# Kernel optimization log

Measured on AMD Instinct MI355X. Metric: run time of the kernel, lower is better.

## Reference

```python
import jax, jax.numpy as jnp
import numpy as np

N_NODES = 100000
N_EDGES = 3200000
D_NODE = 128
D_EDGE = 16


def setup_inputs() -> dict:
    key = jax.random.key(0)
    k1, k2, k3, k4, k5, k6, k7 = jax.random.split(key, 7)
    nodes = jax.random.normal(k1, (N_NODES, D_NODE), dtype=jnp.float32)
    edges = jax.random.normal(k2, (N_EDGES, D_EDGE), dtype=jnp.float32)
    senders = jax.random.randint(k3, (N_EDGES,), 0, N_NODES, dtype=jnp.int32)
    receivers = jax.random.randint(k4, (N_EDGES,), 0, N_NODES, dtype=jnp.int32)
    w_node = jax.random.normal(k5, (), dtype=jnp.float32)
    w_edge = jax.random.normal(k6, (), dtype=jnp.float32)
    b_node = jax.random.normal(k7, (), dtype=jnp.float32)
    return {
        "nodes": nodes,
        "edges": edges,
        "senders": senders,
        "receivers": receivers,
        "w_node": w_node,
        "w_edge": w_edge,
        "b_node": b_node,
    }


def reference(nodes, edges, senders, receivers, w_node, w_edge, b_node):
    # gather sender node scalar feature (column 0): [E]
    sender_vals = nodes[senders, 0]
    edge_vals = edges[:, 0]  # [E]
    # per-edge message: scalar mult-add
    messages = w_edge * edge_vals + w_node * sender_vals  # [E]
    # scatter-add into receivers: [N]
    agg = jax.ops.segment_sum(messages, receivers, num_segments=nodes.shape[0])
    return w_node * nodes[:, 0] + agg + b_node
```

## Files before the change

kernel.cpp:

```cpp
#include <hip/hip_runtime.h>

#define N_NODES 100000
#define N_EDGES 3200000
#define D_NODE 128
#define D_EDGE 16

#define NB 80
#define SLICE_E (N_EDGES / NB)

#define K1_THREADS 512
#define K1_EPT 8
#define K1_TILE (K1_THREADS * K1_EPT)

#define WS_X      0
#define WS_MSG    102400
#define WS_PART   (102400 + N_EDGES)
#define WS_TOTAL  (WS_PART + NB * N_NODES)

__global__ void tmp_k0_extract(const float* __restrict__ nodes,
                               float* __restrict__ x) {
    int i = blockIdx.x * blockDim.x + threadIdx.x;
    if (i < N_NODES) x[i] = nodes[(size_t)i * D_NODE];
}

__global__ __launch_bounds__(K1_THREADS) void tmp_k1_messages(
        const float* __restrict__ x,
        const float* __restrict__ edges,
        const int*   __restrict__ senders,
        const float* __restrict__ w_node,
        const float* __restrict__ w_edge,
        float* __restrict__ msg) {
    const float wn = w_node[0];
    const float we = w_edge[0];
    const int tile = blockIdx.x * K1_TILE;
#pragma unroll
    for (int j = 0; j < K1_EPT; ++j) {
        int e = tile + j * K1_THREADS + (int)threadIdx.x;
        if (e < N_EDGES) {
            float ev = __builtin_nontemporal_load(edges + (size_t)e * D_EDGE);
            int   s  = senders[e];
            msg[e] = we * ev + wn * x[s];
        }
    }
}

__global__ __launch_bounds__(1024) void tmp_k2_accum(
        const float* __restrict__ msg,
        const int*   __restrict__ receivers,
        float* __restrict__ partials,
        int range_floats) {
    extern __shared__ float acc[];
    const int lo   = blockIdx.y * range_floats;
    int span = N_NODES - lo; if (span > range_floats) span = range_floats;
    const unsigned uspan = (unsigned)span;
    const int slice = blockIdx.x;

    for (int i = threadIdx.x; i < span; i += 1024) acc[i] = 0.f;
    __syncthreads();

    const int start = slice * SLICE_E;
    const int end   = start + SLICE_E;
    for (int e = start + (int)threadIdx.x * 4; e < end; e += 1024 * 4) {
        int4   r = *(const int4*)(receivers + e);
        float4 m = *(const float4*)(msg + e);
        unsigned ux = (unsigned)(r.x - lo);
        unsigned uy = (unsigned)(r.y - lo);
        unsigned uz = (unsigned)(r.z - lo);
        unsigned uw = (unsigned)(r.w - lo);
        if (ux < uspan) atomicAdd(&acc[ux], m.x);
        if (uy < uspan) atomicAdd(&acc[uy], m.y);
        if (uz < uspan) atomicAdd(&acc[uz], m.z);
        if (uw < uspan) atomicAdd(&acc[uw], m.w);
    }
    __syncthreads();

    float* dst = partials + (size_t)slice * N_NODES + lo;
    for (int i = threadIdx.x * 4; i < span; i += 1024 * 4) {
        *(float4*)(dst + i) = *(const float4*)(acc + i);
    }
}

__global__ void tmp_k3_reduce(const float* __restrict__ x,
                              const float* __restrict__ partials,
                              const float* __restrict__ w_node,
                              const float* __restrict__ b_node,
                              float* __restrict__ out) {
    int i = blockIdx.x * blockDim.x + threadIdx.x;
    if (i >= N_NODES) return;
    float s = w_node[0] * x[i] + b_node[0];
    const float* p = partials + i;
#pragma unroll 4
    for (int b = 0; b < NB; ++b) s += p[(size_t)b * N_NODES];
    out[i] = s;
}

__global__ void tmp_init_out(const float* __restrict__ nodes,
                             const float* __restrict__ w_node,
                             const float* __restrict__ b_node,
                             float* __restrict__ out) {
    int i = blockIdx.x * blockDim.x + threadIdx.x;
    if (i < N_NODES) out[i] = w_node[0] * nodes[(size_t)i * D_NODE] + b_node[0];
}

__global__ void tmp_edge_scatter_direct(const float* __restrict__ nodes,
                                        const float* __restrict__ edges,
                                        const int*   __restrict__ senders,
                                        const int*   __restrict__ receivers,
                                        const float* __restrict__ w_node,
                                        const float* __restrict__ w_edge,
                                        float* __restrict__ out) {
    const float wn = w_node[0];
    const float we = w_edge[0];
    int base = (blockIdx.x * blockDim.x + threadIdx.x) * 4;
    if (base + 3 < N_EDGES) {
        int4 s = *(const int4*)(senders + base);
        int4 r = *(const int4*)(receivers + base);
        atomicAdd(&out[r.x], we * edges[(size_t)(base + 0) * D_EDGE] + wn * nodes[(size_t)s.x * D_NODE]);
        atomicAdd(&out[r.y], we * edges[(size_t)(base + 1) * D_EDGE] + wn * nodes[(size_t)s.y * D_NODE]);
        atomicAdd(&out[r.z], we * edges[(size_t)(base + 2) * D_EDGE] + wn * nodes[(size_t)s.z * D_NODE]);
        atomicAdd(&out[r.w], we * edges[(size_t)(base + 3) * D_EDGE] + wn * nodes[(size_t)s.w * D_NODE]);
    } else {
        for (int e = base; e < N_EDGES; ++e) {
            atomicAdd(&out[receivers[e]],
                      we * edges[(size_t)e * D_EDGE] + wn * nodes[(size_t)senders[e] * D_NODE]);
        }
    }
}

extern "C" void kernel_launch(void* const* d_in, const int* in_sizes, int n_in,
                              void* d_out, int out_size, void* d_ws, size_t ws_size,
                              hipStream_t stream) {
    const float* nodes     = (const float*)d_in[0];
    const float* edges     = (const float*)d_in[1];
    const int*   senders   = (const int*)d_in[2];
    const int*   receivers = (const int*)d_in[3];
    const float* w_node    = (const float*)d_in[4];
    const float* w_edge    = (const float*)d_in[5];
    const float* b_node    = (const float*)d_in[6];
    float* out = (float*)d_out;
    float* ws  = (float*)d_ws;

    if (ws_size >= (size_t)WS_TOTAL * sizeof(float)) {
        float* x        = ws + WS_X;
        float* msg      = ws + WS_MSG;
        float* partials = ws + WS_PART;

        int range_floats = 40960;
        size_t lds_bytes = (size_t)range_floats * sizeof(float);
        if (hipFuncSetAttribute(reinterpret_cast<const void*>(tmp_k2_accum),
                                hipFuncAttributeMaxDynamicSharedMemorySize,
                                (int)lds_bytes) != hipSuccess) {
            range_floats = 32768;
            lds_bytes = (size_t)range_floats * sizeof(float);
            if (hipFuncSetAttribute(reinterpret_cast<const void*>(tmp_k2_accum),
                                    hipFuncAttributeMaxDynamicSharedMemorySize,
                                    (int)lds_bytes) != hipSuccess) {
                range_floats = 16384;
                lds_bytes = (size_t)range_floats * sizeof(float);
            }
        }
        int n_ranges = (N_NODES + range_floats - 1) / range_floats;

        int threads = 256;
        tmp_k0_extract<<<(N_NODES + threads - 1) / threads, threads, 0, stream>>>(
            nodes, x);

        int k1_blocks = (N_EDGES + K1_TILE - 1) / K1_TILE;
        tmp_k1_messages<<<k1_blocks, K1_THREADS, 0, stream>>>(
            x, edges, senders, w_node, w_edge, msg);

        dim3 grid2(NB, n_ranges);
        tmp_k2_accum<<<grid2, 1024, lds_bytes, stream>>>(
            msg, receivers, partials, range_floats);

        tmp_k3_reduce<<<(N_NODES + threads - 1) / threads, threads, 0, stream>>>(
            x, partials, w_node, b_node, out);
    } else {
        int threads = 256;
        tmp_init_out<<<(N_NODES + threads - 1) / threads, threads, 0, stream>>>(
            nodes, w_node, b_node, out);
        int n_thr = N_EDGES / 4;
        tmp_edge_scatter_direct<<<(n_thr + threads - 1) / threads, threads, 0, stream>>>(
            nodes, edges, senders, receivers, w_node, w_edge, out);
    }
}
```

Baseline: 367.7 us.

## Fuse message and scatter into one kernel with global atomics into replicated partials

Replaces the message-materialization kernel and the LDS range-partitioned accumulation with a single edge kernel. It computes each message and atomically adds it into one of 8 global partial copies chosen by block index, then a reduce kernel sums the 8 copies. This drops the msg buffer write/read, the 80×N partials array and the repeated receiver scans across ranges. In exchange it relies on global float atomics with random addresses, which may suffer contention and L2 atomic throughput limits.

```diff
diff --git a/kernel.cpp b/kernel.cpp
--- a/kernel.cpp
+++ b/kernel.cpp
@@ -5,92 +5,70 @@
 #define D_NODE 128
 #define D_EDGE 16
 
-#define NB 80
-#define SLICE_E (N_EDGES / NB)
-
-#define K1_THREADS 512
-#define K1_EPT 8
-#define K1_TILE (K1_THREADS * K1_EPT)
+#define NPART 8
 
 #define WS_X      0
-#define WS_MSG    102400
-#define WS_PART   (102400 + N_EDGES)
-#define WS_TOTAL  (WS_PART + NB * N_NODES)
+#define WS_PART   102400
+#define WS_TOTAL  (WS_PART + NPART * N_NODES)
 
-__global__ void tmp_k0_extract(const float* __restrict__ nodes,
-                               float* __restrict__ x) {
+#define E_THREADS 256
+#define E_EPT     4
+
+typedef int   iv4 __attribute__((ext_vector_type(4)));
+typedef float fv4 __attribute__((ext_vector_type(4)));
+
+__global__ void v2_init(const float* __restrict__ nodes,
+                        float* __restrict__ x,
+                        float* __restrict__ part) {
     int i = blockIdx.x * blockDim.x + threadIdx.x;
-    if (i < N_NODES) x[i] = nodes[(size_t)i * D_NODE];
+    if (i < NPART * N_NODES) part[i] = 0.f;
+    if (i < N_NODES)         x[i] = nodes[(size_t)i * D_NODE];
 }
 
-__global__ __launch_bounds__(K1_THREADS) void tmp_k1_messages(
+__global__ __launch_bounds__(E_THREADS) void v2_edges(
         const float* __restrict__ x,
         const float* __restrict__ edges,
         const int*   __restrict__ senders,
+        const int*   __restrict__ receivers,
         const float* __restrict__ w_node,
         const float* __restrict__ w_edge,
-        float* __restrict__ msg) {
+        float* __restrict__ part) {
     const float wn = w_node[0];
     const float we = w_edge[0];
-    const int tile = blockIdx.x * K1_TILE;
-#pragma unroll
-    for (int j = 0; j < K1_EPT; ++j) {
-        int e = tile + j * K1_THREADS + (int)threadIdx.x;
-        if (e < N_EDGES) {
-            float ev = __builtin_nontemporal_load(edges + (size_t)e * D_EDGE);
-            int   s  = senders[e];
-            msg[e] = we * ev + wn * x[s];
+
+    float* p = part + (size_t)(blockIdx.x & (NPART - 1)) * N_NODES;
+
+    const int base = (blockIdx.x * E_THREADS + (int)threadIdx.x) * E_EPT;
+    if (base + E_EPT - 1 < N_EDGES) {
+        iv4 s = __builtin_nontemporal_load((const iv4*)(senders + base));
+        iv4 r = __builtin_nontemporal_load((const iv4*)(receivers + base));
+        float e0 = __builtin_nontemporal_load(edges + (size_t)(base + 0) * D_EDGE);
+        float e1 = __builtin_nontemporal_load(edges + (size_t)(base + 1) * D_EDGE);
+        float e2 = __builtin_nontemporal_load(edges + (size_t)(base + 2) * D_EDGE);
+        float e3 = __builtin_nontemporal_load(edges + (size_t)(base + 3) * D_EDGE);
+        float x0 = x[s.x], x1 = x[s.y], x2 = x[s.z], x3 = x[s.w];
+        atomicAdd(&p[r.x], we * e0 + wn * x0);
+        atomicAdd(&p[r.y], we * e1 + wn * x1);
+        atomicAdd(&p[r.z], we * e2 + wn * x2);
+        atomicAdd(&p[r.w], we * e3 + wn * x3);
+    } else {
+        for (int e = base; e < N_EDGES; ++e) {
+            float ev = edges[(size_t)e * D_EDGE];
+            atomicAdd(&p[receivers[e]], we * ev + wn * x[senders[e]]);
         }
     }
 }
 
-__global__ __launch_bounds__(1024) void tmp_k2_accum(
-        const float* __restrict__ msg,
-        const int*   __restrict__ receivers,
-        float* __restrict__ partials,
-        int range_floats) {
-    extern __shared__ float acc[];
-    const int lo   = blockIdx.y * range_floats;
-    int span = N_NODES - lo; if (span > range_floats) span = range_floats;
-    const unsigned uspan = (unsigned)span;
-    const int slice = blockIdx.x;
-
-    for (int i = threadIdx.x; i < span; i += 1024) acc[i] = 0.f;
-    __syncthreads();
-
-    const int start = slice * SLICE_E;
-    const int end   = start + SLICE_E;
-    for (int e = start + (int)threadIdx.x * 4; e < end; e += 1024 * 4) {
-        int4   r = *(const int4*)(receivers + e);
-        float4 m = *(const float4*)(msg + e);
-        unsigned ux = (unsigned)(r.x - lo);
-        unsigned uy = (unsigned)(r.y - lo);
-        unsigned uz = (unsigned)(r.z - lo);
-        unsigned uw = (unsigned)(r.w - lo);
-        if (ux < uspan) atomicAdd(&acc[ux], m.x);
-        if (uy < uspan) atomicAdd(&acc[uy], m.y);
-        if (uz < uspan) atomicAdd(&acc[uz], m.z);
-        if (uw < uspan) atomicAdd(&acc[uw], m.w);
-    }
-    __syncthreads();
-
-    float* dst = partials + (size_t)slice * N_NODES + lo;
-    for (int i = threadIdx.x * 4; i < span; i += 1024 * 4) {
-        *(float4*)(dst + i) = *(const float4*)(acc + i);
-    }
-}
-
-__global__ void tmp_k3_reduce(const float* __restrict__ x,
-                              const float* __restrict__ partials,
-                              const float* __restrict__ w_node,
-                              const float* __restrict__ b_node,
-                              float* __restrict__ out) {
+__global__ void v2_out(const float* __restrict__ x,
+                       const float* __restrict__ part,
+                       const float* __restrict__ w_node,
+                       const float* __restrict__ b_node,
+                       float* __restrict__ out) {
     int i = blockIdx.x * blockDim.x + threadIdx.x;
     if (i >= N_NODES) return;
     float s = w_node[0] * x[i] + b_node[0];
-    const float* p = partials + i;
-#pragma unroll 4
-    for (int b = 0; b < NB; ++b) s += p[(size_t)b * N_NODES];
+#pragma unroll
+    for (int c = 0; c < NPART; ++c) s += part[(size_t)c * N_NODES + i];
     out[i] = s;
 }
 
@@ -113,8 +91,8 @@
     const float we = w_edge[0];
     int base = (blockIdx.x * blockDim.x + threadIdx.x) * 4;
     if (base + 3 < N_EDGES) {
-        int4 s = *(const int4*)(senders + base);
-        int4 r = *(const int4*)(receivers + base);
+        iv4 s = *(const iv4*)(senders + base);
+        iv4 r = *(const iv4*)(receivers + base);
         atomicAdd(&out[r.x], we * edges[(size_t)(base + 0) * D_EDGE] + wn * nodes[(size_t)s.x * D_NODE]);
         atomicAdd(&out[r.y], we * edges[(size_t)(base + 1) * D_EDGE] + wn * nodes[(size_t)s.y * D_NODE]);
         atomicAdd(&out[r.z], we * edges[(size_t)(base + 2) * D_EDGE] + wn * nodes[(size_t)s.z * D_NODE]);
@@ -141,40 +119,20 @@
     float* ws  = (float*)d_ws;
 
     if (ws_size >= (size_t)WS_TOTAL * sizeof(float)) {
-        float* x        = ws + WS_X;
-        float* msg      = ws + WS_MSG;
-        float* partials = ws + WS_PART;
-
-        int range_floats = 40960;
-        size_t lds_bytes = (size_t)range_floats * sizeof(float);
-        if (hipFuncSetAttribute(reinterpret_cast<const void*>(tmp_k2_accum),
-                                hipFuncAttributeMaxDynamicSharedMemorySize,
-                                (int)lds_bytes) != hipSuccess) {
-            range_floats = 32768;
-            lds_bytes = (size_t)range_floats * sizeof(float);
-            if (hipFuncSetAttribute(reinterpret_cast<const void*>(tmp_k2_accum),
-                                    hipFuncAttributeMaxDynamicSharedMemorySize,
-                                    (int)lds_bytes) != hipSuccess) {
-                range_floats = 16384;
-                lds_bytes = (size_t)range_floats * sizeof(float);
-            }
-        }
-        int n_ranges = (N_NODES + range_floats - 1) / range_floats;
+        float* x    = ws + WS_X;
+        float* part = ws + WS_PART;
 
         int threads = 256;
-        tmp_k0_extract<<<(N_NODES + threads - 1) / threads, threads, 0, stream>>>(
-            nodes, x);
+        int init_n  = NPART * N_NODES;
+        v2_init<<<(init_n + threads - 1) / threads, threads, 0, stream>>>(
+            nodes, x, part);
 
-        int k1_blocks = (N_EDGES + K1_TILE - 1) / K1_TILE;
-        tmp_k1_messages<<<k1_blocks, K1_THREADS, 0, stream>>>(
-            x, edges, senders, w_node, w_edge, msg);
+        int e_blocks = N_EDGES / (E_THREADS * E_EPT);
+        v2_edges<<<e_blocks, E_THREADS, 0, stream>>>(
+            x, edges, senders, receivers, w_node, w_edge, part);
 
-        dim3 grid2(NB, n_ranges);
-        tmp_k2_accum<<<grid2, 1024, lds_bytes, stream>>>(
-            msg, receivers, partials, range_floats);
-
-        tmp_k3_reduce<<<(N_NODES + threads - 1) / threads, threads, 0, stream>>>(
-            x, partials, w_node, b_node, out);
+        v2_out<<<(N_NODES + threads - 1) / threads, threads, 0, stream>>>(
+            x, part, w_node, b_node, out);
     } else {
         int threads = 256;
         tmp_init_out<<<(N_NODES + threads - 1) / threads, threads, 0, stream>>>(
```

New measurement: 440.8 us. +19.9%, slower.
